# Performance work log

Measured on AMD Instinct MI355X. Metric: run time of the kernel, lower is better.

The kernel has to match this reference:

```python
import jax, jax.numpy as jnp
import numpy as np

B, N_CAM, J = 8, 5, 15        # batch, cameras, joints
H, W = 128, 240               # heatmap h, w  (HEATMAP_SIZE = [240, 128] = [w, h])
VX, VY, VZ = 80, 80, 20       # voxels_per_axis
NBINS = VX * VY * VZ          # 128000


def setup_inputs() -> dict:
    key = jax.random.key(0)
    k1, k2 = jax.random.split(key)
    heatmaps = jax.random.uniform(k1, (B, N_CAM, J, H, W), dtype=jnp.float32)
    # cached projected sampling grid, clamped to [-1.1, 1.1] as in project_grid
    sample_grid = jax.random.uniform(k2, (N_CAM, NBINS, 2), dtype=jnp.float32,
                                     minval=-1.1, maxval=1.1)
    return {"heatmaps": heatmaps, "sample_grid": sample_grid}


def _grid_sample_bilinear(hm, grid):
    """F.grid_sample(mode='bilinear', padding_mode='zeros', align_corners=True).

    hm:   [B, n, J, H, W]
    grid: [n, nbins, 2]  normalized (x, y) in roughly [-1.1, 1.1]
    returns [B, n, J, nbins]
    """
    Bv, n, Jv, Hv, Wv = hm.shape
    nb = grid.shape[1]
    gx, gy = grid[..., 0], grid[..., 1]
    # align_corners=True mapping from [-1, 1] to pixel coords
    ix = (gx + 1.0) * 0.5 * (Wv - 1)
    iy = (gy + 1.0) * 0.5 * (Hv - 1)
    x0 = jnp.floor(ix)
    y0 = jnp.floor(iy)
    x1 = x0 + 1.0
    y1 = y0 + 1.0
    wx1 = ix - x0
    wx0 = 1.0 - wx1
    wy1 = iy - y0
    wy0 = 1.0 - wy1

    hmf = hm.reshape(Bv, n, Jv, Hv * Wv)

    def gather(yi, xi):
        # zeros padding: out-of-range corners contribute 0
        valid = ((xi >= 0) & (xi <= Wv - 1) & (yi >= 0) & (yi <= Hv - 1))
        xc = jnp.clip(xi, 0, Wv - 1).astype(jnp.int32)
        yc = jnp.clip(yi, 0, Hv - 1).astype(jnp.int32)
        idx = yc * Wv + xc                                   # [n, nb]
        idxb = jnp.broadcast_to(idx[None, :, None, :], (Bv, n, Jv, nb))
        vals = jnp.take_along_axis(hmf, idxb, axis=3)        # [B, n, J, nb]
        return vals * valid[None, :, None, :].astype(hm.dtype)

    out = (gather(y0, x0) * (wy0 * wx0)[None, :, None, :]
           + gather(y0, x1) * (wy0 * wx1)[None, :, None, :]
           + gather(y1, x0) * (wy1 * wx0)[None, :, None, :]
           + gather(y1, x1) * (wy1 * wx1)[None, :, None, :])
    return out


def reference(heatmaps, sample_grid):
    sampled = _grid_sample_bilinear(heatmaps, sample_grid)   # [B, n, J, nbins]
    cubes = jnp.clip(jnp.mean(sampled, axis=1), 0.0, 1.0)    # mean over cameras
    return cubes.reshape(heatmaps.shape[0], heatmaps.shape[2], VX, VY, VZ)
```

## Files before the change

### kernel.cpp

```cpp
#include <hip/hip_runtime.h>
#include <hip/hip_fp16.h>

#define B_     8
#define NCAM   5
#define J_     15
#define H_     128
#define W_     240
#define NB     128000
#define HW_    (H_ * W_)
#define OV_ROWS (H_ - 1)
#define OV_DW   (OV_ROWS * W_)
#define OV_G4   (OV_DW / 4)
#define TPB    1024
#define NCHUNK 8
#define BPB    (NB / NCHUNK)
#define ITEMS  16
#define NBJ    (B_ * J_)
#define NBLK   (NBJ * NCHUNK)

typedef __fp16 fp16x2 __attribute__((ext_vector_type(2)));

__device__ __forceinline__ unsigned int pkrtz(float lo, float hi) {
    fp16x2 h = __builtin_amdgcn_cvt_pkrtz(lo, hi);
    return __builtin_bit_cast(unsigned int, h);
}

__device__ __forceinline__ float fdot2(unsigned int d, unsigned int w, float c) {
#if __has_builtin(__builtin_amdgcn_fdot2)
    return __builtin_amdgcn_fdot2(__builtin_bit_cast(fp16x2, d),
                                  __builtin_bit_cast(fp16x2, w), c, false);
#else
    __half2 p = __hmul2(__builtin_bit_cast(__half2, d),
                        __builtin_bit_cast(__half2, w));
    return c + __low2float(p) + __high2float(p);
#endif
}

__device__ __forceinline__ void bilinear_rec(float gx, float gy,
                                             unsigned int& addr,
                                             unsigned int& w0pk,
                                             unsigned int& w1pk) {
    const float ix = (gx + 1.0f) * (0.5f * (W_ - 1));
    const float iy = (gy + 1.0f) * (0.5f * (H_ - 1));
    const float x0f = floorf(ix);
    const float y0f = floorf(iy);
    const float wx1 = ix - x0f, wx0 = 1.0f - wx1;
    const float wy1 = iy - y0f, wy0 = 1.0f - wy1;
    const int x0 = (int)x0f;
    const int y0 = (int)y0f;
    const int xc = min(max(x0, 0), W_ - 2);
    const int yc = min(max(y0, 0), H_ - 2);
    const float vx0 = (x0 >= 0  && x0 <= W_ - 1) ? wx0 : 0.0f;
    const float vx1 = (x0 >= -1 && x0 <= W_ - 2) ? wx1 : 0.0f;
    const float vy0 = (y0 >= 0  && y0 <= H_ - 1) ? wy0 : 0.0f;
    const float vy1 = (y0 >= -1 && y0 <= H_ - 2) ? wy1 : 0.0f;
    const bool xhi = (x0 == W_ - 1);
    const bool xlo = (x0 == -1);
    const bool yhi = (y0 == H_ - 1);
    const bool ylo = (y0 == -1);
    const float a0 = (xhi ? 0.0f : vx0) + (xlo ? vx1 : 0.0f);
    const float a1 = (xhi ? vx0 : 0.0f) + (xlo ? 0.0f : vx1);
    const float b0 = (yhi ? 0.0f : vy0) + (ylo ? vy1 : 0.0f);
    const float b1 = (yhi ? vy0 : 0.0f) + (ylo ? 0.0f : vy1);
    addr = (unsigned int)(yc * W_ + xc);
    w0pk = pkrtz(0.2f * (a0 * b0), 0.2f * (a0 * b1));
    w1pk = pkrtz(0.2f * (a1 * b0), 0.2f * (a1 * b1));
}

__global__ __launch_bounds__(256) void weights_kernel(
    const float* __restrict__ sgrid,
    unsigned short* __restrict__ addr16,
    uint2* __restrict__ wpk)
{
    const int i = blockIdx.x * 256 + threadIdx.x;
    if (i >= NCAM * NB) return;
    const float2 g = ((const float2*)sgrid)[i];
    unsigned int a, w0, w1;
    bilinear_rec(g.x, g.y, a, w0, w1);
    addr16[i] = (unsigned short)a;
    wpk[i] = make_uint2(w0, w1);
}

__device__ __forceinline__ void stage_overlap(const float* __restrict__ img,
                                              unsigned int* s_img, int tid) {
    const float4* __restrict__ src4 = (const float4*)img;
    uint4* dst = (uint4*)s_img;
    for (int gi = tid; gi < OV_G4; gi += TPB) {
        const int y  = gi / 60;
        const int xg = gi - y * 60;
        const float4 t = src4[y * 60 + xg];
        const float4 b = src4[y * 60 + 60 + xg];
        uint4 d;
        d.x = pkrtz(t.x, b.x);
        d.y = pkrtz(t.y, b.y);
        d.z = pkrtz(t.z, b.z);
        d.w = pkrtz(t.w, b.w);
        dst[gi] = d;
    }
}

#define LOADI(IT) \
    const unsigned int a##IT = ap[(IT) * TPB + tid]; \
    const uint2        w##IT = wp[(IT) * TPB + tid];
#define LOADI_T(IT) \
    const int rt##IT = min((IT) * TPB + tid, BPB - 1); \
    const unsigned int a##IT = ap[rt##IT]; \
    const uint2        wt##IT = wp[rt##IT]; \
    const uint2        w##IT = tail_ok ? wt##IT : make_uint2(0u, 0u);
#define DSI(IT) \
    const unsigned int p##IT = s_img[a##IT]; \
    const unsigned int q##IT = s_img[a##IT + 1u];
#define DOTI(IT) \
    acc##IT = fdot2(q##IT, w##IT.y, fdot2(p##IT, w##IT.x, acc##IT));
#define OUTI(IT) \
    if ((IT) * TPB + tid < BPB) \
        o[(IT) * TPB + tid] = fminf(fmaxf(acc##IT, 0.0f), 1.0f);

__global__ __launch_bounds__(TPB, 4) void project_kernel(
    const float* __restrict__ hm,
    const unsigned short* __restrict__ addr16,
    const uint2* __restrict__ wpk,
    float* __restrict__ out,
    int bpb)
{
    __shared__ unsigned int s_img[OV_DW];
    const int tid   = threadIdx.x;
    const int bj    = blockIdx.x % NBJ;
    const int chunk = blockIdx.x / NBJ;
    const int b     = bj / J_;
    const int j     = bj % J_;
    const int bin0  = chunk * BPB;
    const bool tail_ok = (tid < BPB - (ITEMS - 1) * TPB);

    float acc0 = 0.f, acc1 = 0.f, acc2 = 0.f, acc3 = 0.f;
    float acc4 = 0.f, acc5 = 0.f, acc6 = 0.f, acc7 = 0.f;
    float acc8 = 0.f, acc9 = 0.f, acc10 = 0.f, acc11 = 0.f;
    float acc12 = 0.f, acc13 = 0.f, acc14 = 0.f, acc15 = 0.f;

    for (int n = 0; n < NCAM; ++n) {
        const unsigned short* __restrict__ ap = addr16 + n * NB + bin0;
        const uint2* __restrict__ wp = wpk + n * NB + bin0;
        LOADI(0) LOADI(1) LOADI(2) LOADI(3)
        __syncthreads();
        stage_overlap(hm + (((size_t)b * NCAM + n) * J_ + j) * HW_, s_img, tid);
        __syncthreads();
        if (tid < bpb) {
            LOADI(4) LOADI(5) LOADI(6) LOADI(7)
            DSI(0) DSI(1) DSI(2) DSI(3)
            DOTI(0) DOTI(1) DOTI(2) DOTI(3)
            if (4 * TPB + tid < bpb) {
                LOADI(8) LOADI(9) LOADI(10) LOADI(11)
                DSI(4) DSI(5) DSI(6) DSI(7)
                DOTI(4) DOTI(5) DOTI(6) DOTI(7)
                if (8 * TPB + tid < bpb) {
                    LOADI(12) LOADI(13) LOADI(14) LOADI_T(15)
                    DSI(8) DSI(9) DSI(10) DSI(11)
                    DOTI(8) DOTI(9) DOTI(10) DOTI(11)
                    if (12 * TPB + tid < bpb) {
                        DSI(12) DSI(13) DSI(14) DSI(15)
                        DOTI(12) DOTI(13) DOTI(14) DOTI(15)
                    }
                }
            }
        }
    }

    float* __restrict__ o = out + (size_t)bj * NB + bin0;
    OUTI(0) OUTI(1) OUTI(2) OUTI(3) OUTI(4) OUTI(5) OUTI(6) OUTI(7)
    OUTI(8) OUTI(9) OUTI(10) OUTI(11) OUTI(12) OUTI(13) OUTI(14) OUTI(15)
}

#define FB_SMEM   (HW_ * 4)
#define FB_NCHUNK 5
#define FB_BPB    (NB / FB_NCHUNK)
#define FB_ITEMS  (FB_BPB / TPB)
__global__ __launch_bounds__(TPB) void project_fallback(
    const float* __restrict__ hm,
    const float* __restrict__ sgrid,
    float* __restrict__ out)
{
    extern __shared__ float s_f32[];
    const int tid   = threadIdx.x;
    const int bj    = blockIdx.x % NBJ;
    const int chunk = blockIdx.x / NBJ;
    const int b     = bj / J_;
    const int j     = bj % J_;
    const int bin0  = chunk * FB_BPB;

    float acc[FB_ITEMS];
#pragma unroll
    for (int it = 0; it < FB_ITEMS; ++it) acc[it] = 0.0f;

    for (int n = 0; n < NCAM; ++n) {
        __syncthreads();
        const float4* __restrict__ src =
            (const float4*)(hm + (((size_t)b * NCAM + n) * J_ + j) * HW_);
        float4* dst = (float4*)s_f32;
        for (int i = tid; i < HW_ / 4; i += TPB) dst[i] = src[i];
        __syncthreads();
        const float2* __restrict__ g2 = (const float2*)sgrid + n * NB + bin0;
#pragma unroll
        for (int it = 0; it < FB_ITEMS; ++it) {
            const float2 g = g2[it * TPB + tid];
            const float ix = (g.x + 1.0f) * (0.5f * (W_ - 1));
            const float iy = (g.y + 1.0f) * (0.5f * (H_ - 1));
            const float x0f = floorf(ix), y0f = floorf(iy);
            const float wx1 = ix - x0f, wx0 = 1.0f - wx1;
            const float wy1 = iy - y0f, wy0 = 1.0f - wy1;
            const int x0 = (int)x0f, y0 = (int)y0f;
            const int xc = min(max(x0, 0), W_ - 2);
            const int yc = min(max(y0, 0), H_ - 2);
            const float vx0 = (x0 >= 0  && x0 <= W_ - 1) ? wx0 : 0.0f;
            const float vx1 = (x0 >= -1 && x0 <= W_ - 2) ? wx1 : 0.0f;
            const float vy0 = (y0 >= 0  && y0 <= H_ - 1) ? wy0 : 0.0f;
            const float vy1 = (y0 >= -1 && y0 <= H_ - 2) ? wy1 : 0.0f;
            const bool xhi = (x0 == W_ - 1), xlo = (x0 == -1);
            const bool yhi = (y0 == H_ - 1), ylo = (y0 == -1);
            const float a0 = (xhi ? 0.0f : vx0) + (xlo ? vx1 : 0.0f);
            const float a1 = (xhi ? vx0 : 0.0f) + (xlo ? 0.0f : vx1);
            const float b0 = (yhi ? 0.0f : vy0) + (ylo ? vy1 : 0.0f);
            const float b1 = (yhi ? vy0 : 0.0f) + (ylo ? 0.0f : vy1);
            const float* r0 = s_f32 + (yc * W_ + xc);
            acc[it] += b0 * (a0 * r0[0] + a1 * r0[1])
                     + b1 * (a0 * r0[W_] + a1 * r0[W_ + 1]);
        }
    }
    float* __restrict__ o = out + (size_t)bj * NB + bin0;
#pragma unroll
    for (int it = 0; it < FB_ITEMS; ++it)
        o[it * TPB + tid] = fminf(fmaxf(acc[it] * 0.2f, 0.0f), 1.0f);
}

extern "C" void kernel_launch(void* const* d_in, const int* in_sizes, int n_in,
                              void* d_out, int out_size, void* d_ws, size_t ws_size,
                              hipStream_t stream) {
    const float* hm = (const float*)d_in[0];
    const float* sg = (const float*)d_in[1];
    float* out = (float*)d_out;

    (void)hipFuncSetAttribute((const void*)project_fallback,
                              hipFuncAttributeMaxDynamicSharedMemorySize, FB_SMEM);

    const size_t addr_bytes = (size_t)NCAM * NB * sizeof(unsigned short);
    const size_t wpk_bytes  = (size_t)NCAM * NB * sizeof(uint2);
    if (ws_size >= addr_bytes + wpk_bytes) {
        unsigned short* addr16 = (unsigned short*)d_ws;
        uint2* wpk = (uint2*)((char*)d_ws + addr_bytes);
        weights_kernel<<<(NCAM * NB + 255) / 256, 256, 0, stream>>>(sg, addr16, wpk);
        project_kernel<<<NBLK, TPB, 0, stream>>>(hm, addr16, wpk, out, BPB);
    } else {
        project_fallback<<<NBJ * FB_NCHUNK, TPB, FB_SMEM, stream>>>(hm, sg, out);
    }
}
```

Before: 227.0 us.

## Double-buffer heatmap staging in LDS with pair-packed layout and perm-based gather

Replaces the per-camera row-overlap fp16 staging with a horizontally pair-packed fp16 image held in two LDS buffers, so the next camera's heatmap is staged while the current camera's bins are gathered and accumulated. This removes one of the two barriers per camera and hides global-load latency behind the LDS gather work. Addresses now encode a parity bit: odd x positions need extra LDS reads plus v_perm byte selects to rebuild the pixel pairs, and the weights are regrouped to match. LDS use roughly doubles, which can lower occupancy. The deeply nested tid<bpb guards that gate staging look fragile, because staging work only runs when a thread also has bins to process.

```diff
diff --git a/kernel.cpp b/kernel.cpp
--- a/kernel.cpp
+++ b/kernel.cpp
@@ -8,9 +8,9 @@
 #define W_     240
 #define NB     128000
 #define HW_    (H_ * W_)
-#define OV_ROWS (H_ - 1)
-#define OV_DW   (OV_ROWS * W_)
-#define OV_G4   (OV_DW / 4)
+#define XP_DW   15360
+#define XP_PAD  15368
+#define XP_G4   (XP_DW / 4)
 #define TPB    1024
 #define NCHUNK 8
 #define BPB    (NB / NCHUNK)
@@ -62,9 +62,11 @@
     const float a1 = (xhi ? vx0 : 0.0f) + (xlo ? 0.0f : vx1);
     const float b0 = (yhi ? 0.0f : vy0) + (ylo ? vy1 : 0.0f);
     const float b1 = (yhi ? vy0 : 0.0f) + (ylo ? 0.0f : vy1);
-    addr = (unsigned int)(yc * W_ + xc);
-    w0pk = pkrtz(0.2f * (a0 * b0), 0.2f * (a0 * b1));
-    w1pk = pkrtz(0.2f * (a1 * b0), 0.2f * (a1 * b1));
+    const int xp = xc >> 1;
+    const int p  = xc & 1;
+    addr = (unsigned int)(yc * 120 + xp) | ((unsigned int)p << 14);
+    w0pk = pkrtz(0.2f * (a0 * b0), 0.2f * (a1 * b0));
+    w1pk = pkrtz(0.2f * (a0 * b1), 0.2f * (a1 * b1));
 }
 
 __global__ __launch_bounds__(256) void weights_kernel(
@@ -81,24 +83,6 @@
     wpk[i] = make_uint2(w0, w1);
 }
 
-__device__ __forceinline__ void stage_overlap(const float* __restrict__ img,
-                                              unsigned int* s_img, int tid) {
-    const float4* __restrict__ src4 = (const float4*)img;
-    uint4* dst = (uint4*)s_img;
-    for (int gi = tid; gi < OV_G4; gi += TPB) {
-        const int y  = gi / 60;
-        const int xg = gi - y * 60;
-        const float4 t = src4[y * 60 + xg];
-        const float4 b = src4[y * 60 + 60 + xg];
-        uint4 d;
-        d.x = pkrtz(t.x, b.x);
-        d.y = pkrtz(t.y, b.y);
-        d.z = pkrtz(t.z, b.z);
-        d.w = pkrtz(t.w, b.w);
-        dst[gi] = d;
-    }
-}
-
 #define LOADI(IT) \
     const unsigned int a##IT = ap[(IT) * TPB + tid]; \
     const uint2        w##IT = wp[(IT) * TPB + tid];
@@ -108,10 +92,28 @@
     const uint2        wt##IT = wp[rt##IT]; \
     const uint2        w##IT = tail_ok ? wt##IT : make_uint2(0u, 0u);
 #define DSI(IT) \
-    const unsigned int p##IT = s_img[a##IT]; \
-    const unsigned int q##IT = s_img[a##IT + 1u];
-#define DOTI(IT) \
-    acc##IT = fdot2(q##IT, w##IT.y, fdot2(p##IT, w##IT.x, acc##IT));
+    const unsigned int pa##IT = a##IT & 0x3FFFu; \
+    const unsigned int d00_##IT = cbuf[pa##IT]; \
+    const unsigned int d10_##IT = cbuf[pa##IT + 120u]; \
+    unsigned int d01_##IT = 0u, d11_##IT = 0u; \
+    if (a##IT >> 14) { d01_##IT = cbuf[pa##IT + 1u]; \
+                       d11_##IT = cbuf[pa##IT + 121u]; }
+#define DOTI(IT) { \
+    const unsigned int sel##IT = 0x03020100u + (a##IT >> 14) * 0x02020202u; \
+    const unsigned int r0##IT = __builtin_amdgcn_perm(d01_##IT, d00_##IT, sel##IT); \
+    const unsigned int r1##IT = __builtin_amdgcn_perm(d11_##IT, d10_##IT, sel##IT); \
+    acc##IT = fdot2(r1##IT, w##IT.y, fdot2(r0##IT, w##IT.x, acc##IT)); }
+#define STAGE_UNIT(K) \
+    if (stage_on && ((K) * TPB + tid < XP_G4)) { \
+        const int gi##K = (K) * TPB + tid; \
+        const int row##K = gi##K / 30; \
+        const int xg##K = gi##K - row##K * 30; \
+        const float4 t0##K = src4[row##K * 60 + 2 * xg##K]; \
+        const float4 t1##K = src4[row##K * 60 + 2 * xg##K + 1]; \
+        nxt4[row##K * 30 + xg##K] = \
+            make_uint4(pkrtz(t0##K.x, t0##K.y), pkrtz(t0##K.z, t0##K.w), \
+                       pkrtz(t1##K.x, t1##K.y), pkrtz(t1##K.z, t1##K.w)); \
+    }
 #define OUTI(IT) \
     if ((IT) * TPB + tid < BPB) \
         o[(IT) * TPB + tid] = fminf(fmaxf(acc##IT, 0.0f), 1.0f);
@@ -123,7 +125,7 @@
     float* __restrict__ out,
     int bpb)
 {
-    __shared__ unsigned int s_img[OV_DW];
+    __shared__ __align__(16) unsigned int s_img[2][XP_PAD];
     const int tid   = threadIdx.x;
     const int bj    = blockIdx.x % NBJ;
     const int chunk = blockIdx.x / NBJ;
@@ -137,32 +139,65 @@
     float acc8 = 0.f, acc9 = 0.f, acc10 = 0.f, acc11 = 0.f;
     float acc12 = 0.f, acc13 = 0.f, acc14 = 0.f, acc15 = 0.f;
 
+    {
+        const float4* __restrict__ s0 =
+            (const float4*)(hm + (((size_t)b * NCAM + 0) * J_ + j) * HW_);
+        uint4* __restrict__ d0 = (uint4*)(&s_img[0][0]);
+        for (int gi = tid; gi < XP_G4; gi += TPB) {
+            const int row = gi / 30;
+            const int xg = gi - row * 30;
+            const float4 t0 = s0[row * 60 + 2 * xg];
+            const float4 t1 = s0[row * 60 + 2 * xg + 1];
+            d0[row * 30 + xg] =
+                make_uint4(pkrtz(t0.x, t0.y), pkrtz(t0.z, t0.w),
+                           pkrtz(t1.x, t1.y), pkrtz(t1.z, t1.w));
+        }
+    }
+    __syncthreads();
+
     for (int n = 0; n < NCAM; ++n) {
         const unsigned short* __restrict__ ap = addr16 + n * NB + bin0;
         const uint2* __restrict__ wp = wpk + n * NB + bin0;
+        const unsigned int* __restrict__ cbuf = &s_img[n & 1][0];
+        uint4* __restrict__ nxt4 = (uint4*)(&s_img[(n + 1) & 1][0]);
+        const bool stage_on = (n < NCAM - 1);
+        const int np = stage_on ? n + 1 : n;
+        const float4* __restrict__ src4 =
+            (const float4*)(hm + (((size_t)b * NCAM + np) * J_ + j) * HW_);
+
         LOADI(0) LOADI(1) LOADI(2) LOADI(3)
-        __syncthreads();
-        stage_overlap(hm + (((size_t)b * NCAM + n) * J_ + j) * HW_, s_img, tid);
-        __syncthreads();
         if (tid < bpb) {
             LOADI(4) LOADI(5) LOADI(6) LOADI(7)
-            DSI(0) DSI(1) DSI(2) DSI(3)
-            DOTI(0) DOTI(1) DOTI(2) DOTI(3)
-            if (4 * TPB + tid < bpb) {
-                LOADI(8) LOADI(9) LOADI(10) LOADI(11)
-                DSI(4) DSI(5) DSI(6) DSI(7)
-                DOTI(4) DOTI(5) DOTI(6) DOTI(7)
-                if (8 * TPB + tid < bpb) {
-                    LOADI(12) LOADI(13) LOADI(14) LOADI_T(15)
-                    DSI(8) DSI(9) DSI(10) DSI(11)
-                    DOTI(8) DOTI(9) DOTI(10) DOTI(11)
-                    if (12 * TPB + tid < bpb) {
-                        DSI(12) DSI(13) DSI(14) DSI(15)
-                        DOTI(12) DOTI(13) DOTI(14) DOTI(15)
+            STAGE_UNIT(0)
+            if (1 * TPB + tid < bpb) {
+                DSI(0) DSI(1) DOTI(0) DOTI(1)
+                DSI(2) DSI(3) DOTI(2) DOTI(3)
+                if (2 * TPB + tid < bpb) {
+                    LOADI(8) LOADI(9) LOADI(10) LOADI(11)
+                    STAGE_UNIT(1)
+                    if (3 * TPB + tid < bpb) {
+                        DSI(4) DSI(5) DOTI(4) DOTI(5)
+                        DSI(6) DSI(7) DOTI(6) DOTI(7)
+                        if (4 * TPB + tid < bpb) {
+                            LOADI(12) LOADI(13) LOADI(14) LOADI_T(15)
+                            STAGE_UNIT(2)
+                            if (5 * TPB + tid < bpb) {
+                                DSI(8) DSI(9) DOTI(8) DOTI(9)
+                                DSI(10) DSI(11) DOTI(10) DOTI(11)
+                                if (6 * TPB + tid < bpb) {
+                                    STAGE_UNIT(3)
+                                    if (7 * TPB + tid < bpb) {
+                                        DSI(12) DSI(13) DOTI(12) DOTI(13)
+                                        DSI(14) DSI(15) DOTI(14) DOTI(15)
+                                    }
+                                }
+                            }
+                        }
                     }
                 }
             }
         }
+        __syncthreads();
     }
 
     float* __restrict__ o = out + (size_t)bj * NB + bin0;
```

After: 211.9 us, median of 2. -6.6%, faster.

## Process two batches per block, packing the batch pair into fp16x2 shared memory

Applied to the files above, without the earlier changes.

Each block now covers a pair of batch items for one joint instead of one. The shared image packs the two batches' pixels as an fp16x2 pair, where before it packed vertically adjacent rows. Each bin does four shared reads plus byte permutes, and the packed weights are reordered to match. This halves the per-output address and weight loads and avoids re-reading each heatmap row twice during staging. In exchange it adds permute ALU work and doubles the number of chunks to keep the block count unchanged.

```diff
diff --git a/kernel.cpp b/kernel.cpp
--- a/kernel.cpp
+++ b/kernel.cpp
@@ -8,15 +8,13 @@
 #define W_     240
 #define NB     128000
 #define HW_    (H_ * W_)
-#define OV_ROWS (H_ - 1)
-#define OV_DW   (OV_ROWS * W_)
-#define OV_G4   (OV_DW / 4)
 #define TPB    1024
-#define NCHUNK 8
+#define NBP    (B_ / 2)
+#define NBPJ   (NBP * J_)
+#define NCHUNK 16
 #define BPB    (NB / NCHUNK)
-#define ITEMS  16
-#define NBJ    (B_ * J_)
-#define NBLK   (NBJ * NCHUNK)
+#define ITEMS  8
+#define NBLK   (NBPJ * NCHUNK)
 
 typedef __fp16 fp16x2 __attribute__((ext_vector_type(2)));
 
@@ -63,8 +61,8 @@
     const float b0 = (yhi ? 0.0f : vy0) + (ylo ? vy1 : 0.0f);
     const float b1 = (yhi ? vy0 : 0.0f) + (ylo ? 0.0f : vy1);
     addr = (unsigned int)(yc * W_ + xc);
-    w0pk = pkrtz(0.2f * (a0 * b0), 0.2f * (a0 * b1));
-    w1pk = pkrtz(0.2f * (a1 * b0), 0.2f * (a1 * b1));
+    w0pk = pkrtz(0.2f * (a0 * b0), 0.2f * (a1 * b0));
+    w1pk = pkrtz(0.2f * (a0 * b1), 0.2f * (a1 * b1));
 }
 
 __global__ __launch_bounds__(256) void weights_kernel(
@@ -81,24 +79,6 @@
     wpk[i] = make_uint2(w0, w1);
 }
 
-__device__ __forceinline__ void stage_overlap(const float* __restrict__ img,
-                                              unsigned int* s_img, int tid) {
-    const float4* __restrict__ src4 = (const float4*)img;
-    uint4* dst = (uint4*)s_img;
-    for (int gi = tid; gi < OV_G4; gi += TPB) {
-        const int y  = gi / 60;
-        const int xg = gi - y * 60;
-        const float4 t = src4[y * 60 + xg];
-        const float4 b = src4[y * 60 + 60 + xg];
-        uint4 d;
-        d.x = pkrtz(t.x, b.x);
-        d.y = pkrtz(t.y, b.y);
-        d.z = pkrtz(t.z, b.z);
-        d.w = pkrtz(t.w, b.w);
-        dst[gi] = d;
-    }
-}
-
 #define LOADI(IT) \
     const unsigned int a##IT = ap[(IT) * TPB + tid]; \
     const uint2        w##IT = wp[(IT) * TPB + tid];
@@ -108,13 +88,21 @@
     const uint2        wt##IT = wp[rt##IT]; \
     const uint2        w##IT = tail_ok ? wt##IT : make_uint2(0u, 0u);
 #define DSI(IT) \
-    const unsigned int p##IT = s_img[a##IT]; \
-    const unsigned int q##IT = s_img[a##IT + 1u];
-#define DOTI(IT) \
-    acc##IT = fdot2(q##IT, w##IT.y, fdot2(p##IT, w##IT.x, acc##IT));
+    const unsigned int d00_##IT = s_img[a##IT]; \
+    const unsigned int d01_##IT = s_img[a##IT + 1u]; \
+    const unsigned int d10_##IT = s_img[a##IT + 240u]; \
+    const unsigned int d11_##IT = s_img[a##IT + 241u];
+#define DOTI(IT) { \
+    const unsigned int r00_##IT = __builtin_amdgcn_perm(d01_##IT, d00_##IT, 0x05040100u); \
+    const unsigned int r01_##IT = __builtin_amdgcn_perm(d01_##IT, d00_##IT, 0x07060302u); \
+    const unsigned int r10_##IT = __builtin_amdgcn_perm(d11_##IT, d10_##IT, 0x05040100u); \
+    const unsigned int r11_##IT = __builtin_amdgcn_perm(d11_##IT, d10_##IT, 0x07060302u); \
+    accA##IT = fdot2(r10_##IT, w##IT.y, fdot2(r00_##IT, w##IT.x, accA##IT)); \
+    accB##IT = fdot2(r11_##IT, w##IT.y, fdot2(r01_##IT, w##IT.x, accB##IT)); }
 #define OUTI(IT) \
-    if ((IT) * TPB + tid < BPB) \
-        o[(IT) * TPB + tid] = fminf(fmaxf(acc##IT, 0.0f), 1.0f);
+    if ((IT) * TPB + tid < BPB) { \
+        oA[(IT) * TPB + tid] = fminf(fmaxf(accA##IT, 0.0f), 1.0f); \
+        oB[(IT) * TPB + tid] = fminf(fmaxf(accB##IT, 0.0f), 1.0f); }
 
 __global__ __launch_bounds__(TPB, 4) void project_kernel(
     const float* __restrict__ hm,
@@ -123,53 +111,64 @@
     float* __restrict__ out,
     int bpb)
 {
-    __shared__ unsigned int s_img[OV_DW];
+    __shared__ unsigned int s_img[HW_];
     const int tid   = threadIdx.x;
-    const int bj    = blockIdx.x % NBJ;
-    const int chunk = blockIdx.x / NBJ;
-    const int b     = bj / J_;
-    const int j     = bj % J_;
+    const int bpj   = blockIdx.x % NBPJ;
+    const int chunk = blockIdx.x / NBPJ;
+    const int bp    = bpj / J_;
+    const int j     = bpj % J_;
+    const int b0    = 2 * bp;
+    const int b1    = 2 * bp + 1;
     const int bin0  = chunk * BPB;
     const bool tail_ok = (tid < BPB - (ITEMS - 1) * TPB);
 
-    float acc0 = 0.f, acc1 = 0.f, acc2 = 0.f, acc3 = 0.f;
-    float acc4 = 0.f, acc5 = 0.f, acc6 = 0.f, acc7 = 0.f;
-    float acc8 = 0.f, acc9 = 0.f, acc10 = 0.f, acc11 = 0.f;
-    float acc12 = 0.f, acc13 = 0.f, acc14 = 0.f, acc15 = 0.f;
+    float accA0 = 0.f, accA1 = 0.f, accA2 = 0.f, accA3 = 0.f;
+    float accA4 = 0.f, accA5 = 0.f, accA6 = 0.f, accA7 = 0.f;
+    float accB0 = 0.f, accB1 = 0.f, accB2 = 0.f, accB3 = 0.f;
+    float accB4 = 0.f, accB5 = 0.f, accB6 = 0.f, accB7 = 0.f;
 
     for (int n = 0; n < NCAM; ++n) {
         const unsigned short* __restrict__ ap = addr16 + n * NB + bin0;
         const uint2* __restrict__ wp = wpk + n * NB + bin0;
-        LOADI(0) LOADI(1) LOADI(2) LOADI(3)
-        __syncthreads();
-        stage_overlap(hm + (((size_t)b * NCAM + n) * J_ + j) * HW_, s_img, tid);
+        LOADI(0) LOADI(1)
+        __syncthreads();
+        {
+            const float4* __restrict__ sA =
+                (const float4*)(hm + (((size_t)b0 * NCAM + n) * J_ + j) * HW_);
+            const float4* __restrict__ sB =
+                (const float4*)(hm + (((size_t)b1 * NCAM + n) * J_ + j) * HW_);
+            uint4* __restrict__ dst4 = (uint4*)s_img;
+            for (int gi = tid; gi < HW_ / 4; gi += TPB) {
+                const float4 ta = sA[gi];
+                const float4 tb = sB[gi];
+                dst4[gi] = make_uint4(pkrtz(ta.x, tb.x), pkrtz(ta.y, tb.y),
+                                      pkrtz(ta.z, tb.z), pkrtz(ta.w, tb.w));
+            }
+        }
         __syncthreads();
         if (tid < bpb) {
-            LOADI(4) LOADI(5) LOADI(6) LOADI(7)
-            DSI(0) DSI(1) DSI(2) DSI(3)
-            DOTI(0) DOTI(1) DOTI(2) DOTI(3)
-            if (4 * TPB + tid < bpb) {
-                LOADI(8) LOADI(9) LOADI(10) LOADI(11)
-                DSI(4) DSI(5) DSI(6) DSI(7)
-                DOTI(4) DOTI(5) DOTI(6) DOTI(7)
-                if (8 * TPB + tid < bpb) {
-                    LOADI(12) LOADI(13) LOADI(14) LOADI_T(15)
-                    DSI(8) DSI(9) DSI(10) DSI(11)
-                    DOTI(8) DOTI(9) DOTI(10) DOTI(11)
-                    if (12 * TPB + tid < bpb) {
-                        DSI(12) DSI(13) DSI(14) DSI(15)
-                        DOTI(12) DOTI(13) DOTI(14) DOTI(15)
+            LOADI(2) LOADI(3)
+            DSI(0) DSI(1) DOTI(0) DOTI(1)
+            if (1 * TPB + tid < bpb) {
+                LOADI(4) LOADI(5)
+                DSI(2) DSI(3) DOTI(2) DOTI(3)
+                if (2 * TPB + tid < bpb) {
+                    LOADI(6) LOADI_T(7)
+                    DSI(4) DSI(5) DOTI(4) DOTI(5)
+                    if (3 * TPB + tid < bpb) {
+                        DSI(6) DSI(7) DOTI(6) DOTI(7)
                     }
                 }
             }
         }
     }
 
-    float* __restrict__ o = out + (size_t)bj * NB + bin0;
+    float* __restrict__ oA = out + ((size_t)(b0 * J_ + j)) * NB + bin0;
+    float* __restrict__ oB = out + ((size_t)(b1 * J_ + j)) * NB + bin0;
     OUTI(0) OUTI(1) OUTI(2) OUTI(3) OUTI(4) OUTI(5) OUTI(6) OUTI(7)
-    OUTI(8) OUTI(9) OUTI(10) OUTI(11) OUTI(12) OUTI(13) OUTI(14) OUTI(15)
-}
-
+}
+
+#define NBJ    (B_ * J_)
 #define FB_SMEM   (HW_ * 4)
 #define FB_NCHUNK 5
 #define FB_BPB    (NB / FB_NCHUNK)
```

Result: no change. 230.3 us (+1.4%).
